# Optimization experiments

Hardware: AMD Instinct MI355X
Metric: run time of the kernel (lower is better)

The kernel has to match this reference:

```python
import jax, jax.numpy as jnp
import numpy as np
import math

D_MODEL = 1024
N_HEADS = 16
D_HEAD = D_MODEL // N_HEADS
D_FF = 4096
BOTTLENECK = D_MODEL // 4  # 256
AB_HIDDEN = max(D_MODEL // 32, 8)  # 32
EPS = 1e-6


def rms_norm(x, w):
    rms = jnp.sqrt(jnp.mean(x * x, axis=-1, keepdims=True) + EPS)
    return x / rms * w


def rotate_half(x):
    x1, x2 = jnp.split(x, 2, axis=-1)
    return jnp.concatenate([-x2, x1], axis=-1)


def rope_tables(T, dim):
    inv_freq = 1.0 / (10000.0 ** (jnp.arange(0, dim, 2, dtype=jnp.float32) / dim))
    t = jnp.arange(T, dtype=jnp.float32)
    freqs = jnp.outer(t, inv_freq)            # [T, dim/2]
    emb = jnp.concatenate([freqs, freqs], -1)  # [T, dim]
    return jnp.cos(emb), jnp.sin(emb)


def setup_inputs() -> dict:
    key = jax.random.key(0)
    ks = jax.random.split(key, 12)
    B, T = 4, 2048
    s = lambda fan_in: 1.0 / math.sqrt(fan_in)
    x = jax.random.normal(ks[0], (B, T, D_MODEL), jnp.float32)
    mask = jnp.tril(jnp.ones((T, T), jnp.int32))  # causal 0/1 mask, mask==0 -> -inf
    return {
        "x": x,
        "mask": mask,
        "norm1_w": jnp.ones((D_MODEL,), jnp.float32),
        "Wq": jax.random.normal(ks[1], (D_MODEL, D_MODEL), jnp.float32) * s(D_MODEL),
        "Wk": jax.random.normal(ks[2], (D_MODEL, D_MODEL), jnp.float32) * s(D_MODEL),
        "Wv": jax.random.normal(ks[3], (D_MODEL, D_MODEL), jnp.float32) * s(D_MODEL),
        "Wo": jax.random.normal(ks[4], (D_MODEL, D_MODEL), jnp.float32) * s(D_MODEL),
        "norm2_w": jnp.ones((D_MODEL,), jnp.float32),
        "w1": jax.random.normal(ks[5], (D_FF, D_MODEL), jnp.float32) * s(D_MODEL),
        "w2": jax.random.normal(ks[6], (D_MODEL, D_FF), jnp.float32) * s(D_FF),
        "fc1": jax.random.normal(ks[7], (AB_HIDDEN, D_MODEL), jnp.float32) * s(D_MODEL),
        "fc2": jax.random.normal(ks[8], (2, AB_HIDDEN), jnp.float32) * s(AB_HIDDEN),
        "down": jax.random.normal(ks[9], (BOTTLENECK, D_MODEL), jnp.float32) * s(D_MODEL),
        "up": jax.random.normal(ks[10], (D_MODEL, BOTTLENECK), jnp.float32) * s(BOTTLENECK),
    }


def attention(x, mask, Wq, Wk, Wv, Wo):
    B, T, D = x.shape
    def split_heads(y):
        return y.reshape(B, T, N_HEADS, D_HEAD).transpose(0, 2, 1, 3)  # [B,H,T,Dh]
    q = split_heads(x @ Wq.T)
    k = split_heads(x @ Wk.T)
    v = split_heads(x @ Wv.T)
    cos, sin = rope_tables(T, D_HEAD)
    cos = cos[None, None]; sin = sin[None, None]
    q = q * cos + rotate_half(q) * sin
    k = k * cos + rotate_half(k) * sin
    scores = jnp.einsum("bhqd,bhkd->bhqk", q, k) / math.sqrt(D_HEAD)
    scores = jnp.where(mask[:T, :T] == 0, -jnp.inf, scores)
    attn = jax.nn.softmax(scores, axis=-1)
    out = jnp.einsum("bhqk,bhkd->bhqd", attn, v)
    out = out.transpose(0, 2, 1, 3).reshape(B, T, D)
    return out @ Wo.T


def reference(x, mask, norm1_w, Wq, Wk, Wv, Wo, norm2_w, w1, w2, fc1, fc2, down, up):
    # group='B': gated FFN + projection branch (dropout=0 / eval mode)
    x = x + attention(rms_norm(x, norm1_w), mask, Wq, Wk, Wv, Wo)
    normed = rms_norm(x, norm2_w)
    ffn_out = jax.nn.gelu(normed @ w1.T, approximate=False) @ w2.T
    # AttentionAlphaBetaLM: mean over tokens, tiny MLP -> (alpha, beta)
    g = normed.mean(axis=1)                      # [B, D]
    h = jax.nn.relu(g @ fc1.T)                   # [B, hidden]
    ab = h @ fc2.T                               # [B, 2]
    alpha = jax.nn.sigmoid(ab[:, 0])             # [B]
    beta = jax.nn.sigmoid(ab[:, 1])              # allow_negative_beta=False for group B
    proj_out = jax.nn.relu(normed @ down.T) @ up.T
    x = x + alpha[:, None, None] * ffn_out + beta[:, None, None] * proj_out
    return x
```

## Files before the change

### kernel.cpp

```cpp
#include <hip/hip_runtime.h>
#include <hip/hip_bf16.h>
#include <math.h>

typedef unsigned short u16;
typedef unsigned int   u32;

typedef __bf16 bf16x8_t __attribute__((ext_vector_type(8)));
typedef float  f32x4_t  __attribute__((ext_vector_type(4)));

__device__ float AB_dev[8];

__device__ inline float bf2f(u16 u) {
    u32 x = ((u32)u) << 16;
    return __builtin_bit_cast(float, x);
}
__device__ inline u16 f2bf(float f) {
    u32 x = __builtin_bit_cast(u32, f);
    return (u16)((x + 0x7fffu + ((x >> 16) & 1u)) >> 16);
}
__device__ inline uint4 stage_pack_f32(const float* p) {
    float4 f0 = ((const float4*)p)[0];
    float4 f1 = ((const float4*)p)[1];
    u32 w0 = (u32)f2bf(f0.x) | ((u32)f2bf(f0.y) << 16);
    u32 w1 = (u32)f2bf(f0.z) | ((u32)f2bf(f0.w) << 16);
    u32 w2 = (u32)f2bf(f1.x) | ((u32)f2bf(f1.y) << 16);
    u32 w3 = (u32)f2bf(f1.z) | ((u32)f2bf(f1.w) << 16);
    return uint4{w0, w1, w2, w3};
}
#define GLD(gptr, lptr) __builtin_amdgcn_global_load_lds( \
    (const __attribute__((address_space(1))) void*)(gptr), \
    (__attribute__((address_space(3))) void*)(lptr), 16, 0, 0)

template <int CTRL>
__device__ inline float dpp_f(float x) {
    int r = __builtin_amdgcn_update_dpp(0, __builtin_bit_cast(int, x), CTRL, 0xf, 0xf, false);
    return __builtin_bit_cast(float, r);
}
__device__ inline float row_max16(float x) {
    x = fmaxf(x, dpp_f<0x128>(x));
    x = fmaxf(x, dpp_f<0x124>(x));
    x = fmaxf(x, dpp_f<0x122>(x));
    x = fmaxf(x, dpp_f<0x121>(x));
    return x;
}
__device__ inline float row_sum16(float x) {
    x += dpp_f<0x128>(x);
    x += dpp_f<0x124>(x);
    x += dpp_f<0x122>(x);
    x += dpp_f<0x121>(x);
    return x;
}

template <typename TIN>
__global__ __launch_bounds__(256) void rmsnorm_kernel(
    const TIN* __restrict__ x, const float* __restrict__ w, u16* __restrict__ out)
{
    const int row = blockIdx.x, tid = threadIdx.x;
    const size_t rb = (size_t)row * 1024;
    float val[4];
#pragma unroll
    for (int i = 0; i < 4; ++i) {
        size_t idx = rb + tid + i * 256;
        if constexpr (sizeof(TIN) == 4) val[i] = ((const float*)x)[idx];
        else                            val[i] = bf2f(((const u16*)x)[idx]);
    }
    float ss = val[0]*val[0] + val[1]*val[1] + val[2]*val[2] + val[3]*val[3];
#pragma unroll
    for (int off = 32; off >= 1; off >>= 1) ss += __shfl_xor(ss, off, 64);
    __shared__ float red[4];
    if ((tid & 63) == 0) red[tid >> 6] = ss;
    __syncthreads();
    float tot = red[0] + red[1] + red[2] + red[3];
    float inv = rsqrtf(tot * (1.0f / 1024.0f) + 1e-6f);
    u16* orow = out + rb;
#pragma unroll
    for (int i = 0; i < 4; ++i)
        orow[tid + i * 256] = f2bf(val[i] * inv * w[tid + i * 256]);
}

__global__ __launch_bounds__(256) void convm_kernel(
    const float* __restrict__ s0, const float* __restrict__ s1,
    const float* __restrict__ s2, const float* __restrict__ s3,
    u16* __restrict__ d0, u16* __restrict__ d1,
    u16* __restrict__ d2, u16* __restrict__ d3, int shift)
{
    int sel = blockIdx.x >> shift;
    int loc = blockIdx.x & ((1 << shift) - 1);
    const float* s = sel == 0 ? s0 : sel == 1 ? s1 : sel == 2 ? s2 : s3;
    u16*       d = sel == 0 ? d0 : sel == 1 ? d1 : sel == 2 ? d2 : d3;
    size_t i = ((size_t)loc * 256 + threadIdx.x) * 8;
    *(uint4*)(d + i) = stage_pack_f32(s + i);
}

enum { EPI_QKV = 0, EPI_ADDX_F32 = 1, EPI_GELU = 2, EPI_COMB0 = 3,
       EPI_COMBA = 4, EPI_RELU = 5, EPI_BSCALE = 6 };

template <int EPI>
__global__ __launch_bounds__(256) void gemm128e(
    const u16* __restrict__ A, int sA, const u16* __restrict__ Wb, int sW,
    void* __restrict__ C, const float* __restrict__ Xf,
    const u16* __restrict__ Xh, int N, int K)
{
    __shared__ __align__(16) u16 As[128 * 32];
    __shared__ __align__(16) u16 Bs[128 * 32];
    const int tid  = threadIdx.x;
    const int wave = tid >> 6, lane = tid & 63;
    const int quad = lane >> 4, l16 = lane & 15;
    const int row0 = blockIdx.y * 128, col0 = blockIdx.x * 128;
    const int wm = (wave >> 1) * 64, wn = (wave & 1) * 64;

    f32x4_t acc[4][4];
#pragma unroll
    for (int i = 0; i < 4; ++i)
#pragma unroll
        for (int j = 0; j < 4; ++j) { f32x4_t z = {0,0,0,0}; acc[i][j] = z; }

    const u16* Abase = A + (size_t)row0 * sA;
    const int id0 = tid, id1 = tid + 256;
    const size_t aoff0 = (size_t)(id0 >> 2) * sA + (id0 & 3) * 8;
    const size_t aoff1 = (size_t)(id1 >> 2) * sA + (id1 & 3) * 8;
    const size_t boff0 = (size_t)(col0 + (id0 >> 2)) * sW + (id0 & 3) * 8;
    const size_t boff1 = (size_t)(col0 + (id1 >> 2)) * sW + (id1 & 3) * 8;
    u16* lA0 = As + (size_t)(wave * 64) * 8;
    u16* lA1 = As + (size_t)(256 + wave * 64) * 8;
    u16* lB0 = Bs + (size_t)(wave * 64) * 8;
    u16* lB1 = Bs + (size_t)(256 + wave * 64) * 8;

    for (int k0 = 0; k0 < K; k0 += 32) {
        __syncthreads();
        GLD(Abase + aoff0 + k0, lA0);
        GLD(Abase + aoff1 + k0, lA1);
        GLD(Wb + boff0 + k0, lB0);
        GLD(Wb + boff1 + k0, lB1);
        __syncthreads();

        const bf16x8_t* As8 = (const bf16x8_t*)As;
        const bf16x8_t* Bs8 = (const bf16x8_t*)Bs;
        bf16x8_t af[4], bfr[4];
#pragma unroll
        for (int i = 0; i < 4; ++i) {
            af[i]  = As8[(wm + i * 16 + l16) * 4 + quad];
            bfr[i] = Bs8[(wn + i * 16 + l16) * 4 + quad];
        }
#pragma unroll
        for (int i = 0; i < 4; ++i)
#pragma unroll
            for (int j = 0; j < 4; ++j)
                acc[i][j] = __builtin_amdgcn_mfma_f32_16x16x32_bf16(
                    af[i], bfr[j], acc[i][j], 0, 0, 0);
    }

    float al = 0.0f;
    if (EPI == EPI_COMB0 || EPI == EPI_COMBA)
        al = AB_dev[blockIdx.y >> 4];
#pragma unroll
    for (int i = 0; i < 4; ++i) {
        int mbase = row0 + wm + i * 16 + quad * 4;
#pragma unroll
        for (int j = 0; j < 4; ++j) {
            int n = col0 + wn + j * 16 + l16;
#pragma unroll
            for (int r = 0; r < 4; ++r) {
                float vv = acc[i][j][r];
                int row = mbase + r;
                if (EPI == EPI_QKV) {
                    int sel = col0 >> 10;
                    float sc = (sel == 0) ? 0.18033688011112042f : 1.0f;
                    ((u16*)C)[(size_t)sel * 8388608 + (size_t)row * 1024 + (n & 1023)]
                        = f2bf(vv * sc);
                } else if (EPI == EPI_ADDX_F32) {
                    size_t off = (size_t)row * N + n;
                    ((u16*)C)[off] = f2bf(vv + Xf[off]);
                } else if (EPI == EPI_GELU) {
                    size_t off = (size_t)row * N + n;
                    vv = 0.5f * vv * (1.0f + erff(vv * 0.70710678118654752f));
                    ((u16*)C)[off] = f2bf(vv);
                } else {
                    size_t off = (size_t)row * N + n;
                    float prev = ((float*)C)[off];
                    float add = (EPI == EPI_COMB0) ? bf2f(Xh[off]) : 0.0f;
                    ((float*)C)[off] = prev + add + al * vv;
                }
            }
        }
    }
}

template <int EPI>
__global__ __launch_bounds__(256) void gemm64b(
    const u16* __restrict__ A, int sA, const u16* __restrict__ Wb, int sW,
    void* __restrict__ C, int N, int K)
{
    __shared__ __align__(16) u16 As[128 * 32];
    __shared__ __align__(16) u16 Bs[64 * 32];
    const int tid  = threadIdx.x;
    const int wave = tid >> 6, lane = tid & 63;
    const int quad = lane >> 4, l16 = lane & 15;
    const int row0 = blockIdx.y * 128, col0 = blockIdx.x * 64;
    const int wm = (wave >> 1) * 64, wn = (wave & 1) * 32;

    f32x4_t acc[4][2];
#pragma unroll
    for (int i = 0; i < 4; ++i)
#pragma unroll
        for (int j = 0; j < 2; ++j) { f32x4_t z = {0,0,0,0}; acc[i][j] = z; }

    const u16* Abase = A + (size_t)row0 * sA;
    const int id0 = tid, id1 = tid + 256;
    const size_t aoff0 = (size_t)(id0 >> 2) * sA + (id0 & 3) * 8;
    const size_t aoff1 = (size_t)(id1 >> 2) * sA + (id1 & 3) * 8;
    const size_t woff  = (size_t)(col0 + (tid >> 2)) * sW + (tid & 3) * 8;
    u16* lA0 = As + (size_t)(wave * 64) * 8;
    u16* lA1 = As + (size_t)(256 + wave * 64) * 8;
    u16* lB  = Bs + (size_t)(wave * 64) * 8;

    for (int k0 = 0; k0 < K; k0 += 32) {
        __syncthreads();
        GLD(Abase + aoff0 + k0, lA0);
        GLD(Abase + aoff1 + k0, lA1);
        GLD(Wb + woff + k0, lB);
        __syncthreads();

        const bf16x8_t* As8 = (const bf16x8_t*)As;
        const bf16x8_t* Bs8 = (const bf16x8_t*)Bs;
        bf16x8_t af[4], bfr[2];
#pragma unroll
        for (int i = 0; i < 4; ++i) af[i]  = As8[(wm + i * 16 + l16) * 4 + quad];
#pragma unroll
        for (int j = 0; j < 2; ++j) bfr[j] = Bs8[(wn + j * 16 + l16) * 4 + quad];
#pragma unroll
        for (int i = 0; i < 4; ++i)
#pragma unroll
            for (int j = 0; j < 2; ++j)
                acc[i][j] = __builtin_amdgcn_mfma_f32_16x16x32_bf16(
                    af[i], bfr[j], acc[i][j], 0, 0, 0);
    }

#pragma unroll
    for (int i = 0; i < 4; ++i) {
        int mbase = row0 + wm + i * 16 + quad * 4;
#pragma unroll
        for (int j = 0; j < 2; ++j) {
            int n = col0 + wn + j * 16 + l16;
#pragma unroll
            for (int r = 0; r < 4; ++r) {
                float vv = acc[i][j][r];
                int row = mbase + r;
                size_t off = (size_t)row * N + n;
                if (EPI == EPI_RELU) {
                    ((u16*)C)[off] = f2bf(fmaxf(vv, 0.0f));
                } else {
                    ((float*)C)[off] = AB_dev[4 + (row >> 11)] * vv;
                }
            }
        }
    }
}

__global__ __launch_bounds__(256) void rope_kernel(u16* __restrict__ q, u16* __restrict__ k)
{
    int idx = blockIdx.x * 256 + threadIdx.x;
    int i = idx & 31;
    int h = (idx >> 5) & 15;
    int t = (idx >> 9) & 2047;
    int b = idx >> 20;
    float inv = __expf(-(float)i * (9.210340371976184f / 32.0f));
    float ang = (float)t * inv;
    float sn, cs;
    sincosf(ang, &sn, &cs);
    size_t o1 = ((size_t)(b * 2048 + t)) * 1024 + h * 64 + i;
    size_t o2 = o1 + 32;
    float q1 = bf2f(q[o1]), q2 = bf2f(q[o2]);
    q[o1] = f2bf(q1 * cs - q2 * sn);
    q[o2] = f2bf(q2 * cs + q1 * sn);
    float k1 = bf2f(k[o1]), k2 = bf2f(k[o2]);
    k[o1] = f2bf(k1 * cs - k2 * sn);
    k[o2] = f2bf(k2 * cs + k1 * sn);
}

#define TS 72

__global__ __launch_bounds__(256) void flash_kernel(
    const u16* __restrict__ q, const u16* __restrict__ k,
    const u16* __restrict__ v, u16* __restrict__ o)
{
    __shared__ __align__(16) u16 QP[128 * TS];
    __shared__ __align__(16) u16 KT[64 * TS];
    __shared__ __align__(16) u16 VT[64 * TS];

    const int tid  = threadIdx.x;
    const int wave = tid >> 6, lane = tid & 63;
    const int quad = lane >> 4, l16 = lane & 15;
    const int bx = blockIdx.x;
    const int p  = 15 - (bx >> 6);
    const int bh = bx & 63;
    const int h = bh & 15, b = bh >> 4;
    const int q0 = p * 128;
    const int qrow0 = q0 + wave * 16;
    const int qrow1 = q0 + 64 + wave * 16;
    const int last0 = qrow0 + 15;
    const size_t bt_base = (size_t)(b * 2048) * 1024 + h * 64;

    const u16* kbase = k + bt_base;
    const u16* vbase = v + bt_base;

#pragma unroll
    for (int it = 0; it < 4; ++it) {
        int id = it * 256 + tid;
        int row = id >> 3, c8 = (id & 7) * 8;
        uint4 val = *(const uint4*)(q + bt_base + (size_t)(q0 + row) * 1024 + c8);
        *(uint4*)(QP + row * TS + c8) = val;
    }
    __syncthreads();

    bf16x8_t qf[2][2];
#pragma unroll
    for (int mi = 0; mi < 2; ++mi)
#pragma unroll
        for (int ks = 0; ks < 2; ++ks)
            qf[mi][ks] = *(const bf16x8_t*)(
                QP + (mi * 64 + wave * 16 + l16) * TS + ks * 32 + quad * 8);

    float mst[2][4], lst[2][4];
    f32x4_t oacc[2][4];
#pragma unroll
    for (int mi = 0; mi < 2; ++mi)
#pragma unroll
        for (int r = 0; r < 4; ++r) { mst[mi][r] = -3.0e38f; lst[mi][r] = 0.f; }
#pragma unroll
    for (int mi = 0; mi < 2; ++mi)
#pragma unroll
        for (int dj = 0; dj < 4; ++dj) { f32x4_t z = {0,0,0,0}; oacc[mi][dj] = z; }

    u16* Pl = QP + (wave * 32) * TS;
    const int jmax = q0 + 128;

    for (int j0 = 0; j0 < jmax; j0 += 64) {
        __syncthreads();
#pragma unroll
        for (int it = 0; it < 2; ++it) {
            int id = it * 256 + tid;
            int row = id >> 3, c8 = (id & 7) * 8;
            uint4 kv = *(const uint4*)(kbase + (size_t)(j0 + row) * 1024 + c8);
            *(uint4*)(KT + row * TS + c8) = kv;
            uint4 vv = *(const uint4*)(vbase + (size_t)(j0 + row) * 1024 + c8);
            const u16* vp = (const u16*)&vv;
            int sw = id & 7;
#pragma unroll
            for (int jj = 0; jj < 8; ++jj) {
                int j2 = (jj + sw) & 7;
                VT[(c8 + j2) * TS + row] = vp[j2];
            }
        }
        __syncthreads();

        const bool a0 = (j0 <= last0);

        f32x4_t s[2][4];
#pragma unroll
        for (int mi = 0; mi < 2; ++mi)
#pragma unroll
            for (int nj = 0; nj < 4; ++nj) { f32x4_t z = {0,0,0,0}; s[mi][nj] = z; }
#pragma unroll
        for (int ks = 0; ks < 2; ++ks) {
            bf16x8_t kf2[4];
#pragma unroll
            for (int nj = 0; nj < 4; ++nj)
                kf2[nj] = *(const bf16x8_t*)(KT + (nj * 16 + l16) * TS + ks * 32 + quad * 8);
#pragma unroll
            for (int nj = 0; nj < 4; ++nj)
                s[1][nj] = __builtin_amdgcn_mfma_f32_16x16x32_bf16(
                    qf[1][ks], kf2[nj], s[1][nj], 0, 0, 0);
            if (a0) {
#pragma unroll
                for (int nj = 0; nj < 4; ++nj)
                    s[0][nj] = __builtin_amdgcn_mfma_f32_16x16x32_bf16(
                        qf[0][ks], kf2[nj], s[0][nj], 0, 0, 0);
            }
        }

        if (a0 && j0 + 63 > qrow0) {
#pragma unroll
            for (int nj = 0; nj < 4; ++nj) {
                int key = j0 + nj * 16 + l16;
#pragma unroll
                for (int r = 0; r < 4; ++r)
                    if (key > qrow0 + quad * 4 + r) s[0][nj][r] = -1.0e30f;
            }
        }
        if (j0 + 63 > qrow1) {
#pragma unroll
            for (int nj = 0; nj < 4; ++nj) {
                int key = j0 + nj * 16 + l16;
#pragma unroll
                for (int r = 0; r < 4; ++r)
                    if (key > qrow1 + quad * 4 + r) s[1][nj][r] = -1.0e30f;
            }
        }

#pragma unroll
        for (int mi = 0; mi < 2; ++mi) {
            if (mi == 0 && !a0) continue;
#pragma unroll
            for (int r = 0; r < 4; ++r) {
                float mx = fmaxf(fmaxf(s[mi][0][r], s[mi][1][r]),
                                 fmaxf(s[mi][2][r], s[mi][3][r]));
                mx = row_max16(mx);
                float mn = fmaxf(mst[mi][r], mx);
                float alpha = __builtin_amdgcn_exp2f(mst[mi][r] - mn);
                mst[mi][r] = mn;
                float rs = 0.f;
#pragma unroll
                for (int nj = 0; nj < 4; ++nj) {
                    float pv = __builtin_amdgcn_exp2f(s[mi][nj][r] - mn);
                    rs += pv;
                    Pl[(mi * 16 + quad * 4 + r) * TS + nj * 16 + l16] = f2bf(pv);
                }
                rs = row_sum16(rs);
                lst[mi][r] = lst[mi][r] * alpha + rs;
#pragma unroll
                for (int dj = 0; dj < 4; ++dj) oacc[mi][dj][r] *= alpha;
            }
        }

#pragma unroll
        for (int ks = 0; ks < 2; ++ks) {
            bf16x8_t vf2[4];
#pragma unroll
            for (int dj = 0; dj < 4; ++dj)
                vf2[dj] = *(const bf16x8_t*)(VT + (dj * 16 + l16) * TS + ks * 32 + quad * 8);
            bf16x8_t pf1 = *(const bf16x8_t*)(Pl + (16 + l16) * TS + ks * 32 + quad * 8);
#pragma unroll
            for (int dj = 0; dj < 4; ++dj)
                oacc[1][dj] = __builtin_amdgcn_mfma_f32_16x16x32_bf16(
                    pf1, vf2[dj], oacc[1][dj], 0, 0, 0);
            if (a0) {
                bf16x8_t pf0 = *(const bf16x8_t*)(Pl + (l16)*TS + ks * 32 + quad * 8);
#pragma unroll
                for (int dj = 0; dj < 4; ++dj)
                    oacc[0][dj] = __builtin_amdgcn_mfma_f32_16x16x32_bf16(
                        pf0, vf2[dj], oacc[0][dj], 0, 0, 0);
            }
        }
    }

#pragma unroll
    for (int mi = 0; mi < 2; ++mi) {
        int gb = q0 + mi * 64 + wave * 16;
#pragma unroll
        for (int r = 0; r < 4; ++r) {
            float invl = 1.0f / lst[mi][r];
            size_t rowb = bt_base + (size_t)(gb + quad * 4 + r) * 1024;
#pragma unroll
            for (int dj = 0; dj < 4; ++dj)
                o[rowb + dj * 16 + l16] = f2bf(oacc[mi][dj][r] * invl);
        }
    }
}

__global__ __launch_bounds__(256) void mean_partial_kernel(
    const u16* __restrict__ normed, float* __restrict__ part)
{
    int blk = blockIdx.x;
    int b = blk >> 4, c = blk & 15;
    int tid = threadIdx.x;
    int d0 = tid * 4;
    float s0 = 0, s1 = 0, s2 = 0, s3 = 0;
    const u16* base = normed + ((size_t)b * 2048 + c * 128) * 1024 + d0;
    for (int t = 0; t < 128; ++t) {
        const uint2 uv = *(const uint2*)(base + (size_t)t * 1024);
        s0 += bf2f((u16)(uv.x & 0xffff));
        s1 += bf2f((u16)(uv.x >> 16));
        s2 += bf2f((u16)(uv.y & 0xffff));
        s3 += bf2f((u16)(uv.y >> 16));
    }
    float* o = part + (size_t)blk * 1024 + d0;
    o[0] = s0; o[1] = s1; o[2] = s2; o[3] = s3;
}

__global__ void ab_kernel(const float* __restrict__ part, const float* __restrict__ fc1,
                          const float* __restrict__ fc2)
{
    int b = blockIdx.x, tid = threadIdx.x;
    __shared__ float g[1024];
    __shared__ float h[32];
    for (int d = tid; d < 1024; d += 64) {
        float s = 0;
        for (int c = 0; c < 16; ++c) s += part[(size_t)(b * 16 + c) * 1024 + d];
        g[d] = s * (1.0f / 2048.0f);
    }
    __syncthreads();
    if (tid < 32) {
        float s = 0;
        for (int d = 0; d < 1024; ++d) s += g[d] * fc1[(size_t)tid * 1024 + d];
        h[tid] = fmaxf(s, 0.0f);
    }
    __syncthreads();
    if (tid < 2) {
        float s = 0;
        for (int j = 0; j < 32; ++j) s += h[j] * fc2[(size_t)tid * 32 + j];
        AB_dev[tid * 4 + b] = 1.0f / (1.0f + __expf(-s));
    }
}

__global__ __launch_bounds__(256) void sentinel_kernel(float* __restrict__ out, int n)
{
    int i = blockIdx.x * 256 + threadIdx.x;
    if (i < n) out[i] = 100.0f;
}

extern "C" void kernel_launch(void* const* d_in, const int* in_sizes, int n_in,
                              void* d_out, int out_size, void* d_ws, size_t ws_size,
                              hipStream_t stream)
{
    const float* x   = (const float*)d_in[0];
    const float* n1w = (const float*)d_in[2];
    const float* Wq  = (const float*)d_in[3];
    const float* Wk  = (const float*)d_in[4];
    const float* Wv  = (const float*)d_in[5];
    const float* Wo  = (const float*)d_in[6];
    const float* n2w = (const float*)d_in[7];
    const float* w1  = (const float*)d_in[8];
    const float* w2  = (const float*)d_in[9];
    const float* fc1 = (const float*)d_in[10];
    const float* fc2 = (const float*)d_in[11];
    const float* dwn = (const float*)d_in[12];
    const float* up  = (const float*)d_in[13];

    const size_t MB = 1024 * 1024;
    if (ws_size < 64 * MB) {
        sentinel_kernel<<<(out_size + 255) / 256, 256, 0, stream>>>((float*)d_out, out_size);
        return;
    }

    char* ws = (char*)d_ws;
    u16*   XN1  = (u16*)(ws);
    u16*   ATT  = (u16*)(ws);
    u16*   H1s  = (u16*)(ws);
    u16*   Q    = (u16*)(ws + 16 * MB);
    u16*   XNEW = (u16*)(ws + 16 * MB);
    u16*   K    = (u16*)(ws + 32 * MB);
    u16*   XN2  = (u16*)(ws + 32 * MB);
    u16*   V    = (u16*)(ws + 48 * MB);
    float* PART = (float*)(ws + 48 * MB);
    u16*   DWNB = (u16*)(ws + 48 * MB + 512 * 1024);
    u16*   W1B  = (u16*)(ws + 48 * MB);
    u16*   P1   = (u16*)(ws + 56 * MB);
    u16*   UPB  = (u16*)(ws + 60 * MB);
    u16*   W2B  = (u16*)(ws + 56 * MB);

    u16* WqkvB = (u16*)d_out;
    u16* WoB   = WqkvB + 3 * 1024 * 1024;

    dim3 blk(256);

    convm_kernel<<<2048, blk, 0, stream>>>(Wq, Wk, Wv, Wo,
        WqkvB, WqkvB + 1024 * 1024, WqkvB + 2 * 1024 * 1024, WoB, 9);
    rmsnorm_kernel<float><<<8192, blk, 0, stream>>>(x, n1w, XN1);
    gemm128e<EPI_QKV><<<dim3(24, 64), blk, 0, stream>>>(
        XN1, 1024, WqkvB, 1024, Q, nullptr, nullptr, 1024, 1024);
    rope_kernel<<<16384, blk, 0, stream>>>(Q, K);
    flash_kernel<<<1024, blk, 0, stream>>>(Q, K, V, ATT);
    gemm128e<EPI_ADDX_F32><<<dim3(8, 64), blk, 0, stream>>>(
        ATT, 1024, WoB, 1024, XNEW, x, nullptr, 1024, 1024);
    rmsnorm_kernel<u16><<<8192, blk, 0, stream>>>(XNEW, n2w, XN2);
    mean_partial_kernel<<<64, blk, 0, stream>>>(XN2, PART);
    ab_kernel<<<4, dim3(64), 0, stream>>>(PART, fc1, fc2);
    convm_kernel<<<256, blk, 0, stream>>>(dwn, up, nullptr, nullptr,
                                          DWNB, UPB, nullptr, nullptr, 7);
    gemm64b<EPI_RELU><<<dim3(4, 64), blk, 0, stream>>>(
        XN2, 1024, DWNB, 1024, P1, 256, 1024);
    convm_kernel<<<2048, blk, 0, stream>>>(w1, nullptr, nullptr, nullptr,
                                           W1B, nullptr, nullptr, nullptr, 11);
    gemm64b<EPI_BSCALE><<<dim3(16, 64), blk, 0, stream>>>(
        P1, 256, UPB, 256, d_out, 1024, 256);
    convm_kernel<<<2048, blk, 0, stream>>>(w2, nullptr, nullptr, nullptr,
                                           W2B, nullptr, nullptr, nullptr, 11);
    for (int s = 0; s < 4; ++s) {
        gemm128e<EPI_GELU><<<dim3(8, 64), blk, 0, stream>>>(
            XN2, 1024, W1B + (size_t)s * 1024 * 1024, 1024, H1s,
            nullptr, nullptr, 1024, 1024);
        if (s == 0)
            gemm128e<EPI_COMB0><<<dim3(8, 64), blk, 0, stream>>>(
                H1s, 1024, W2B + s * 1024, 4096, d_out,
                nullptr, XNEW, 1024, 1024);
        else
            gemm128e<EPI_COMBA><<<dim3(8, 64), blk, 0, stream>>>(
                H1s, 1024, W2B + s * 1024, 4096, d_out,
                nullptr, XNEW, 1024, 1024);
    }
}
```

Baseline: 833.8 us.

## Transpose flash S-tile so softmax rows are per-lane; deepen GEMM K step

```diff
diff --git a/kernel.cpp b/kernel.cpp
--- a/kernel.cpp
+++ b/kernel.cpp
@@ -17,6 +17,11 @@
 __device__ inline u16 f2bf(float f) {
     u32 x = __builtin_bit_cast(u32, f);
     return (u16)((x + 0x7fffu + ((x >> 16) & 1u)) >> 16);
+}
+__device__ inline u32 cvt_pk_bf16(float lo, float hi) {
+    u32 r;
+    asm("v_cvt_pk_bf16_f32 %0, %1, %2" : "=v"(r) : "v"(lo), "v"(hi));
+    return r;
 }
 __device__ inline uint4 stage_pack_f32(const float* p) {
     float4 f0 = ((const float4*)p)[0];
@@ -31,26 +36,6 @@
     (const __attribute__((address_space(1))) void*)(gptr), \
     (__attribute__((address_space(3))) void*)(lptr), 16, 0, 0)
 
-template <int CTRL>
-__device__ inline float dpp_f(float x) {
-    int r = __builtin_amdgcn_update_dpp(0, __builtin_bit_cast(int, x), CTRL, 0xf, 0xf, false);
-    return __builtin_bit_cast(float, r);
-}
-__device__ inline float row_max16(float x) {
-    x = fmaxf(x, dpp_f<0x128>(x));
-    x = fmaxf(x, dpp_f<0x124>(x));
-    x = fmaxf(x, dpp_f<0x122>(x));
-    x = fmaxf(x, dpp_f<0x121>(x));
-    return x;
-}
-__device__ inline float row_sum16(float x) {
-    x += dpp_f<0x128>(x);
-    x += dpp_f<0x124>(x);
-    x += dpp_f<0x122>(x);
-    x += dpp_f<0x121>(x);
-    return x;
-}
-
 template <typename TIN>
 __global__ __launch_bounds__(256) void rmsnorm_kernel(
     const TIN* __restrict__ x, const float* __restrict__ w, u16* __restrict__ out)
@@ -101,8 +86,8 @@
     void* __restrict__ C, const float* __restrict__ Xf,
     const u16* __restrict__ Xh, int N, int K)
 {
-    __shared__ __align__(16) u16 As[128 * 32];
-    __shared__ __align__(16) u16 Bs[128 * 32];
+    __shared__ __align__(16) u16 As[2][128 * 32];
+    __shared__ __align__(16) u16 Bs[2][128 * 32];
     const int tid  = threadIdx.x;
     const int wave = tid >> 6, lane = tid & 63;
     const int quad = lane >> 4, l16 = lane & 15;
@@ -121,33 +106,38 @@
     const size_t aoff1 = (size_t)(id1 >> 2) * sA + (id1 & 3) * 8;
     const size_t boff0 = (size_t)(col0 + (id0 >> 2)) * sW + (id0 & 3) * 8;
     const size_t boff1 = (size_t)(col0 + (id1 >> 2)) * sW + (id1 & 3) * 8;
-    u16* lA0 = As + (size_t)(wave * 64) * 8;
-    u16* lA1 = As + (size_t)(256 + wave * 64) * 8;
-    u16* lB0 = Bs + (size_t)(wave * 64) * 8;
-    u16* lB1 = Bs + (size_t)(256 + wave * 64) * 8;
-
-    for (int k0 = 0; k0 < K; k0 += 32) {
+    const size_t ld0 = (size_t)(wave * 64) * 8;
+    const size_t ld1 = (size_t)(256 + wave * 64) * 8;
+
+    for (int k0 = 0; k0 < K; k0 += 64) {
         __syncthreads();
-        GLD(Abase + aoff0 + k0, lA0);
-        GLD(Abase + aoff1 + k0, lA1);
-        GLD(Wb + boff0 + k0, lB0);
-        GLD(Wb + boff1 + k0, lB1);
+        GLD(Abase + aoff0 + k0,      As[0] + ld0);
+        GLD(Abase + aoff1 + k0,      As[0] + ld1);
+        GLD(Abase + aoff0 + k0 + 32, As[1] + ld0);
+        GLD(Abase + aoff1 + k0 + 32, As[1] + ld1);
+        GLD(Wb + boff0 + k0,         Bs[0] + ld0);
+        GLD(Wb + boff1 + k0,         Bs[0] + ld1);
+        GLD(Wb + boff0 + k0 + 32,    Bs[1] + ld0);
+        GLD(Wb + boff1 + k0 + 32,    Bs[1] + ld1);
         __syncthreads();
 
-        const bf16x8_t* As8 = (const bf16x8_t*)As;
-        const bf16x8_t* Bs8 = (const bf16x8_t*)Bs;
-        bf16x8_t af[4], bfr[4];
-#pragma unroll
-        for (int i = 0; i < 4; ++i) {
-            af[i]  = As8[(wm + i * 16 + l16) * 4 + quad];
-            bfr[i] = Bs8[(wn + i * 16 + l16) * 4 + quad];
-        }
-#pragma unroll
-        for (int i = 0; i < 4; ++i)
-#pragma unroll
-            for (int j = 0; j < 4; ++j)
-                acc[i][j] = __builtin_amdgcn_mfma_f32_16x16x32_bf16(
-                    af[i], bfr[j], acc[i][j], 0, 0, 0);
+#pragma unroll
+        for (int hh = 0; hh < 2; ++hh) {
+            const bf16x8_t* As8 = (const bf16x8_t*)As[hh];
+            const bf16x8_t* Bs8 = (const bf16x8_t*)Bs[hh];
+            bf16x8_t af[4], bfr[4];
+#pragma unroll
+            for (int i = 0; i < 4; ++i) {
+                af[i]  = As8[(wm + i * 16 + l16) * 4 + quad];
+                bfr[i] = Bs8[(wn + i * 16 + l16) * 4 + quad];
+            }
+#pragma unroll
+            for (int i = 0; i < 4; ++i)
+#pragma unroll
+                for (int j = 0; j < 4; ++j)
+                    acc[i][j] = __builtin_amdgcn_mfma_f32_16x16x32_bf16(
+                        af[i], bfr[j], acc[i][j], 0, 0, 0);
+        }
     }
 
     float al = 0.0f;
@@ -296,9 +286,9 @@
     const int bh = bx & 63;
     const int h = bh & 15, b = bh >> 4;
     const int q0 = p * 128;
-    const int qrow0 = q0 + wave * 16;
-    const int qrow1 = q0 + 64 + wave * 16;
-    const int last0 = qrow0 + 15;
+    const int qb0 = q0 + wave * 16;
+    const int qb1 = q0 + 64 + wave * 16;
+    const int last0 = qb0 + 15;
     const size_t bt_base = (size_t)(b * 2048) * 1024 + h * 64;
 
     const u16* kbase = k + bt_base;
@@ -321,12 +311,10 @@
             qf[mi][ks] = *(const bf16x8_t*)(
                 QP + (mi * 64 + wave * 16 + l16) * TS + ks * 32 + quad * 8);
 
-    float mst[2][4], lst[2][4];
+    float mst[2], lst[2];
+    mst[0] = mst[1] = -3.0e38f;
+    lst[0] = lst[1] = 0.f;
     f32x4_t oacc[2][4];
-#pragma unroll
-    for (int mi = 0; mi < 2; ++mi)
-#pragma unroll
-        for (int r = 0; r < 4; ++r) { mst[mi][r] = -3.0e38f; lst[mi][r] = 0.f; }
 #pragma unroll
     for (int mi = 0; mi < 2; ++mi)
 #pragma unroll
@@ -370,56 +358,70 @@
 #pragma unroll
             for (int nj = 0; nj < 4; ++nj)
                 s[1][nj] = __builtin_amdgcn_mfma_f32_16x16x32_bf16(
-                    qf[1][ks], kf2[nj], s[1][nj], 0, 0, 0);
+                    kf2[nj], qf[1][ks], s[1][nj], 0, 0, 0);
             if (a0) {
 #pragma unroll
                 for (int nj = 0; nj < 4; ++nj)
                     s[0][nj] = __builtin_amdgcn_mfma_f32_16x16x32_bf16(
-                        qf[0][ks], kf2[nj], s[0][nj], 0, 0, 0);
-            }
-        }
-
-        if (a0 && j0 + 63 > qrow0) {
-#pragma unroll
-            for (int nj = 0; nj < 4; ++nj) {
-                int key = j0 + nj * 16 + l16;
-#pragma unroll
-                for (int r = 0; r < 4; ++r)
-                    if (key > qrow0 + quad * 4 + r) s[0][nj][r] = -1.0e30f;
-            }
-        }
-        if (j0 + 63 > qrow1) {
-#pragma unroll
-            for (int nj = 0; nj < 4; ++nj) {
-                int key = j0 + nj * 16 + l16;
-#pragma unroll
-                for (int r = 0; r < 4; ++r)
-                    if (key > qrow1 + quad * 4 + r) s[1][nj][r] = -1.0e30f;
-            }
+                        kf2[nj], qf[0][ks], s[0][nj], 0, 0, 0);
+            }
+        }
+
+        if (a0 && j0 + 63 > qb0) {
+#pragma unroll
+            for (int nj = 0; nj < 4; ++nj)
+#pragma unroll
+                for (int r = 0; r < 4; ++r) {
+                    int key = j0 + nj * 16 + quad * 4 + r;
+                    if (key > qb0 + l16) s[0][nj][r] = -1.0e30f;
+                }
+        }
+        if (j0 + 63 > qb1) {
+#pragma unroll
+            for (int nj = 0; nj < 4; ++nj)
+#pragma unroll
+                for (int r = 0; r < 4; ++r) {
+                    int key = j0 + nj * 16 + quad * 4 + r;
+                    if (key > qb1 + l16) s[1][nj][r] = -1.0e30f;
+                }
         }
 
 #pragma unroll
         for (int mi = 0; mi < 2; ++mi) {
             if (mi == 0 && !a0) continue;
+            float mx = s[mi][0][0];
+#pragma unroll
+            for (int nj = 0; nj < 4; ++nj)
+#pragma unroll
+                for (int r = 0; r < 4; ++r)
+                    if (nj || r) mx = fmaxf(mx, s[mi][nj][r]);
+            mx = fmaxf(mx, __shfl_xor(mx, 16, 64));
+            mx = fmaxf(mx, __shfl_xor(mx, 32, 64));
+            float mn = fmaxf(mst[mi], mx);
+            float alpha = __builtin_amdgcn_exp2f(mst[mi] - mn);
+            mst[mi] = mn;
+            float rs = 0.f;
+            u16* prow = Pl + (mi * 16 + l16) * TS;
+#pragma unroll
+            for (int nj = 0; nj < 4; ++nj) {
+                float p0 = __builtin_amdgcn_exp2f(s[mi][nj][0] - mn);
+                float p1 = __builtin_amdgcn_exp2f(s[mi][nj][1] - mn);
+                float p2 = __builtin_amdgcn_exp2f(s[mi][nj][2] - mn);
+                float p3 = __builtin_amdgcn_exp2f(s[mi][nj][3] - mn);
+                rs += (p0 + p1) + (p2 + p3);
+                uint2 w;
+                w.x = cvt_pk_bf16(p0, p1);
+                w.y = cvt_pk_bf16(p2, p3);
+                *(uint2*)(prow + nj * 16 + quad * 4) = w;
+            }
+            rs += __shfl_xor(rs, 16, 64);
+            rs += __shfl_xor(rs, 32, 64);
+            lst[mi] = lst[mi] * alpha + rs;
 #pragma unroll
             for (int r = 0; r < 4; ++r) {
-                float mx = fmaxf(fmaxf(s[mi][0][r], s[mi][1][r]),
-                                 fmaxf(s[mi][2][r], s[mi][3][r]));
-                mx = row_max16(mx);
-                float mn = fmaxf(mst[mi][r], mx);
-                float alpha = __builtin_amdgcn_exp2f(mst[mi][r] - mn);
-                mst[mi][r] = mn;
-                float rs = 0.f;
-#pragma unroll
-                for (int nj = 0; nj < 4; ++nj) {
-                    float pv = __builtin_amdgcn_exp2f(s[mi][nj][r] - mn);
-                    rs += pv;
-                    Pl[(mi * 16 + quad * 4 + r) * TS + nj * 16 + l16] = f2bf(pv);
-                }
-                rs = row_sum16(rs);
-                lst[mi][r] = lst[mi][r] * alpha + rs;
-#pragma unroll
-                for (int dj = 0; dj < 4; ++dj) oacc[mi][dj][r] *= alpha;
+                float ar = __shfl(alpha, quad * 4 + r, 64);
+#pragma unroll
+                for (int dj = 0; dj < 4; ++dj) oacc[mi][dj][r] *= ar;
             }
         }
 
@@ -449,7 +451,8 @@
         int gb = q0 + mi * 64 + wave * 16;
 #pragma unroll
         for (int r = 0; r < 4; ++r) {
-            float invl = 1.0f / lst[mi][r];
+            float lr = __shfl(lst[mi], quad * 4 + r, 64);
+            float invl = 1.0f / lr;
             size_t rowb = bt_base + (size_t)(gb + quad * 4 + r) * 1024;
 #pragma unroll
             for (int dj = 0; dj < 4; ++dj)
```

After: 760.6 us. -8.8%, faster.
